# Kernel optimization log

Measured on AMD Instinct MI355X. Metric: run time of the kernel, lower is better.

The kernel has to match this reference:

```python
import jax, jax.numpy as jnp
import numpy as np

# ---- static config (matches init_kwargs) ----
B, CIN, H, W = 32, 64, 32, 32
CO, K, G, PAD = 64, 7, 8, 3
R_RAMP = 3.0            # ramp size R
Z_INIT = 4.0            # initial adaptive-span value
MAXSZ = W // 2          # adaptive_mask max_size = image_size/2 = 16
CPG = CO // G           # channels per group


def _unfold(t, k):
    # torch x.unfold(2,k,1).unfold(3,k,1): [B,C,Hp,Wp] -> [B,C,Ho,Wo,kh,kw]
    ho = t.shape[2] - k + 1
    wo = t.shape[3] - k + 1
    return jnp.stack(
        [jnp.stack([t[:, :, i:i + ho, j:j + wo] for j in range(k)], axis=-1)
         for i in range(k)], axis=-2)


def _adaptive_mask(current_val):
    # AdaptiveMask.forward applied to [B,G,CPG,H,W]; x.shape[-1] == W.
    # one_d_mask[g, i] is the soft value written on 'ring' i (rows i and W-1-i,
    # columns spanning the ring interval) of a WxW mask.
    template = jnp.linspace(1.0 - MAXSZ, 0.0, MAXSZ)            # [MAXSZ]
    om = (template[None, :] + current_val * MAXSZ) / R_RAMP + 1.0
    om = jnp.clip(om, 0.0, 1.0)                                  # [G, MAXSZ]
    # (slice [-(W//2):] is identity since MAXSZ == W//2)
    i = jnp.arange(W)
    r = jnp.minimum(i, W - 1 - i)                                # ring index per row
    top = i <= (W - 1 - i)
    lo = jnp.where(top, r, r + 1)    # bottom row of ring misses its leftmost col
    hi = W - 1 - r
    c = jnp.arange(W)
    in_ring = (c[None, :] >= lo[:, None]) & (c[None, :] <= hi[:, None])  # [W,W]
    vals = om[:, r]                                              # [G, W]
    return jnp.where(in_ring[None, :, :], vals[:, :, None], 1.0)  # [G,W,W]


def setup_inputs() -> dict:
    key = jax.random.key(0)
    ks = jax.random.split(key, 6)
    x = jax.random.normal(ks[0], (B, CIN, H, W), dtype=jnp.float32)
    fan_out_std = np.sqrt(2.0 / CO).astype(np.float32)  # kaiming fan_out, 1x1 conv
    w_q = jax.random.normal(ks[1], (CO, CIN), dtype=jnp.float32) * fan_out_std
    w_k = jax.random.normal(ks[2], (CO, CIN), dtype=jnp.float32) * fan_out_std
    w_v = jax.random.normal(ks[3], (CO, CIN), dtype=jnp.float32) * fan_out_std
    rel_h = jax.random.normal(ks[4], (CO // 2, 1, 1, K, 1), dtype=jnp.float32)
    rel_w = jax.random.normal(ks[5], (CO // 2, 1, 1, 1, K), dtype=jnp.float32)
    current_val = jnp.full((G, 1), Z_INIT, dtype=jnp.float32)
    return {"x": x, "w_q": w_q, "w_k": w_k, "w_v": w_v,
            "rel_h": rel_h, "rel_w": rel_w, "current_val": current_val}


def reference(x, w_q, w_k, w_v, rel_h, rel_w, current_val):
    q = jnp.einsum('bchw,oc->bohw', x, w_q)                       # [B,CO,H,W]
    xp = jnp.pad(x, ((0, 0), (0, 0), (PAD, PAD), (PAD, PAD)))
    k = jnp.einsum('bchw,oc->bohw', xp, w_k)
    v = jnp.einsum('bchw,oc->bohw', xp, w_v)
    k = _unfold(k, K)                                             # [B,CO,H,W,K,K]
    v = _unfold(v, K)
    k_h, k_w = jnp.split(k, 2, axis=1)
    k = jnp.concatenate([k_h + rel_h, k_w + rel_w], axis=1)
    k = k.reshape(B, G, CPG, H, W, K * K)
    v = v.reshape(B, G, CPG, H, W, K * K)
    q = q.reshape(B, G, CPG, H, W, 1)
    scores = jnp.sum(q * k, axis=2)                               # [B,G,H,W,K*K]
    attn = jax.nn.softmax(scores, axis=-1)
    out = jnp.sum(attn[:, :, None] * v, axis=-1)                  # [B,G,CPG,H,W]
    mask = _adaptive_mask(current_val)                            # [G,W,W]
    return out * mask[None, :, None, :, :]
```

## Files before the change

### kernel.cpp

```cpp
#include <hip/hip_runtime.h>

#define BB    32
#define CINc  64
#define HHc   32
#define WWc   32
#define COc   64
#define KSc   7
#define GGc   8
#define PADc  3
#define CPGc  8
#define NPIX  (HHc * WWc)
#define TILEH 8
#define HALOH (TILEH + 6)
#define HALOW (WWc + 6)
#define NPOS  (HALOH * HALOW)

typedef _Float16 half2v __attribute__((ext_vector_type(2)));

#if defined(__has_builtin)
#if __has_builtin(__builtin_amdgcn_fdot2)
#define HAVE_FDOT2 1
#endif
#endif

__global__ __launch_bounds__(256, 6) void fused_kernel(
    const float* __restrict__ x,
    const float* __restrict__ wq,
    const float* __restrict__ wk,
    const float* __restrict__ wv,
    const float* __restrict__ rel_h,
    const float* __restrict__ rel_w,
    const float* __restrict__ cv,
    float* __restrict__ out)
{
    __shared__ __attribute__((aligned(16))) float4 kpl[NPOS];
    __shared__ __attribute__((aligned(16))) float4 vpl0[NPOS];
    __shared__ __attribute__((aligned(16))) float4 vpl1[NPOS];

    const int bi   = blockIdx.x;
    const int xcd  = bi & 7;
    const int sIdx = bi >> 3;
    const int im   = sIdx >> 5;
    const int j    = sIdx & 31;
    const int b    = im * 8 + xcd;
    const int g    = j >> 2;
    const int tile = j & 3;
    const int o0   = g * CPGc;
    const int tid  = threadIdx.x;

    const int y0  = tile * TILEH - PADc;
    const int yv0 = (y0 < 0) ? 0 : y0;
    const int yv1 = (y0 + HALOH - 1 > HHc - 1) ? (HHc - 1) : (y0 + HALOH - 1);
    const int nvp = ((yv1 - yv0) + 1) << 5;
    const int r0  = yv0 - y0;
    const float* xb = x + (size_t)b * CINc * NPIX;

    {
        const float4 z = {0.f, 0.f, 0.f, 0.f};
        for (int p = tid; p < NPOS; p += 256) {
            kpl[p] = z; vpl0[p] = z; vpl1[p] = z;
        }
    }
    __syncthreads();

#pragma unroll 1
    for (int i = tid; i < nvp; i += 256) {
        const int row = i >> 5;
        const int xx  = i & 31;
        const int y   = yv0 + row;
        const float* xp = xb + y * WWc + xx;

        float ak[CPGc], av[CPGc];
#pragma unroll
        for (int oi = 0; oi < CPGc; ++oi) { ak[oi] = 0.f; av[oi] = 0.f; }

        for (int c0 = 0; c0 < CINc; c0 += 8) {
            float xv[8];
#pragma unroll
            for (int jj = 0; jj < 8; ++jj)
                xv[jj] = xp[(c0 + jj) * NPIX];
#pragma unroll
            for (int oi = 0; oi < CPGc; ++oi) {
                const float* wkr = wk + (o0 + oi) * CINc + c0;
                const float* wvr = wv + (o0 + oi) * CINc + c0;
#pragma unroll
                for (int jj = 0; jj < 8; ++jj) {
                    ak[oi] = fmaf(xv[jj], wkr[jj], ak[oi]);
                    av[oi] = fmaf(xv[jj], wvr[jj], av[oi]);
                }
            }
        }

        const int p = (r0 + row) * HALOW + (xx + PADc);
        float4 kst;
        half2v* kp = (half2v*)&kst;
#pragma unroll
        for (int jj = 0; jj < 4; ++jj)
            kp[jj] = half2v{(_Float16)ak[2 * jj], (_Float16)ak[2 * jj + 1]};
        kpl[p]  = kst;
        vpl0[p] = (float4){av[0], av[1], av[2], av[3]};
        vpl1[p] = (float4){av[4], av[5], av[6], av[7]};
    }

    const int w  = tid & 31;
    const int lh = tid >> 5;
    const int h  = tile * TILEH + lh;
    const int poff = h * WWc + w;

    float q[CPGc];
#pragma unroll
    for (int oi = 0; oi < CPGc; ++oi) q[oi] = 0.f;

    for (int c0 = 0; c0 < CINc; c0 += 8) {
        float xv[8];
#pragma unroll
        for (int jj = 0; jj < 8; ++jj)
            xv[jj] = xb[(c0 + jj) * NPIX + poff];
#pragma unroll
        for (int oi = 0; oi < CPGc; ++oi) {
            const float* wqr = wq + (o0 + oi) * CINc + c0;
#pragma unroll
            for (int jj = 0; jj < 8; ++jj)
                q[oi] = fmaf(xv[jj], wqr[jj], q[oi]);
        }
    }

#if HAVE_FDOT2
    half2v q2[4];
#pragma unroll
    for (int jj = 0; jj < 4; ++jj)
        q2[jj] = half2v{(_Float16)q[2 * jj], (_Float16)q[2 * jj + 1]};
#endif

    const bool use_h = (g < 4);
    const float* relp = use_h ? (rel_h + o0 * KSc) : (rel_w + (o0 - 32) * KSc);
    float qrel[KSc];
#pragma unroll
    for (int tt = 0; tt < KSc; ++tt) {
        float s = 0.f;
#pragma unroll
        for (int oi = 0; oi < CPGc; ++oi)
            s = fmaf(q[oi], relp[oi * KSc + tt], s);
        qrel[tt] = s;
    }

    __syncthreads();

    float den = 0.f;
    float acc[CPGc];
#pragma unroll
    for (int oi = 0; oi < CPGc; ++oi) acc[oi] = 0.f;

#pragma unroll
    for (int ki = 0; ki < KSc; ++ki) {
        const int rbase = (lh + ki) * HALOW + w;
#pragma unroll
        for (int kj = 0; kj < KSc; ++kj) {
            const int p = rbase + kj;
            const float4 kraw = kpl[p];
            const float4 v0   = vpl0[p];
            const float4 v1   = vpl1[p];

            float s = use_h ? qrel[ki] : qrel[kj];
#if HAVE_FDOT2
            const half2v* kh = (const half2v*)&kraw;
            s = __builtin_amdgcn_fdot2(q2[0], kh[0], s, false);
            s = __builtin_amdgcn_fdot2(q2[1], kh[1], s, false);
            s = __builtin_amdgcn_fdot2(q2[2], kh[2], s, false);
            s = __builtin_amdgcn_fdot2(q2[3], kh[3], s, false);
#else
            const half2v* kh = (const half2v*)&kraw;
#pragma unroll
            for (int jj = 0; jj < 4; ++jj) {
                s = fmaf(q[2 * jj],     (float)kh[jj].x, s);
                s = fmaf(q[2 * jj + 1], (float)kh[jj].y, s);
            }
#endif
            const float e = __expf(s);
            den += e;
            acc[0] = fmaf(e, v0.x, acc[0]); acc[1] = fmaf(e, v0.y, acc[1]);
            acc[2] = fmaf(e, v0.z, acc[2]); acc[3] = fmaf(e, v0.w, acc[3]);
            acc[4] = fmaf(e, v1.x, acc[4]); acc[5] = fmaf(e, v1.y, acc[5]);
            acc[6] = fmaf(e, v1.z, acc[6]); acc[7] = fmaf(e, v1.w, acc[7]);
        }
    }

    const int  r  = min(h, HHc - 1 - h);
    const int  lo = (h <= HHc - 1 - h) ? r : r + 1;
    const int  hi = HHc - 1 - r;
    const bool in_ring = (w >= lo) && (w <= hi);
    const float cvg = cv[g];
    float om = ((float)r - 15.0f + cvg * 16.0f) * (1.0f / 3.0f) + 1.0f;
    om = fminf(fmaxf(om, 0.0f), 1.0f);
    const float maskv = in_ring ? om : 1.0f;
    const float scale = maskv / den;

    float* ob = out + ((size_t)b * COc + o0) * NPIX + poff;
#pragma unroll
    for (int oi = 0; oi < CPGc; ++oi)
        ob[(size_t)oi * NPIX] = acc[oi] * scale;
}

extern "C" void kernel_launch(void* const* d_in, const int* in_sizes, int n_in,
                              void* d_out, int out_size, void* d_ws, size_t ws_size,
                              hipStream_t stream) {
    const float* x     = (const float*)d_in[0];
    const float* wq    = (const float*)d_in[1];
    const float* wk    = (const float*)d_in[2];
    const float* wv    = (const float*)d_in[3];
    const float* rel_h = (const float*)d_in[4];
    const float* rel_w = (const float*)d_in[5];
    const float* cv    = (const float*)d_in[6];
    float* out = (float*)d_out;

    fused_kernel<<<1024, 256, 0, stream>>>(x, wq, wk, wv, rel_h, rel_w, cv, out);
}
```

Measured before the change: 106.7 us.

## Process whole image per block to drop halo recompute of K/V projections

Each block now covers a full 32x32 image for one (batch, group) pair with 1024 threads, instead of an 8-row tile plus a 3-row halo. Each thread computes its pixel's Q, K and V projections in a single pass, so halo rows are no longer recomputed and the zeroed halo shared buffer goes away. Out-of-bounds neighbours are handled by clamping indices and masking the dot product and value accumulation. The trade-off is fewer blocks (256), which may leave compute units underused, plus extra select instructions in the inner loop.

```diff
diff --git a/kernel.cpp b/kernel.cpp
--- a/kernel.cpp
+++ b/kernel.cpp
@@ -10,10 +10,6 @@
 #define PADc  3
 #define CPGc  8
 #define NPIX  (HHc * WWc)
-#define TILEH 8
-#define HALOH (TILEH + 6)
-#define HALOW (WWc + 6)
-#define NPOS  (HALOH * HALOW)
 
 typedef _Float16 half2v __attribute__((ext_vector_type(2)));
 
@@ -23,7 +19,7 @@
 #endif
 #endif
 
-__global__ __launch_bounds__(256, 6) void fused_kernel(
+__global__ __launch_bounds__(1024, 4) void fused_kernel(
     const float* __restrict__ x,
     const float* __restrict__ wq,
     const float* __restrict__ wk,
@@ -33,103 +29,63 @@
     const float* __restrict__ cv,
     float* __restrict__ out)
 {
-    __shared__ __attribute__((aligned(16))) float4 kpl[NPOS];
-    __shared__ __attribute__((aligned(16))) float4 vpl0[NPOS];
-    __shared__ __attribute__((aligned(16))) float4 vpl1[NPOS];
+    __shared__ __attribute__((aligned(16))) float4 kpl[NPIX];
+    __shared__ __attribute__((aligned(16))) float4 vpl0[NPIX];
+    __shared__ __attribute__((aligned(16))) float4 vpl1[NPIX];
 
-    const int bi   = blockIdx.x;
-    const int xcd  = bi & 7;
-    const int sIdx = bi >> 3;
-    const int im   = sIdx >> 5;
-    const int j    = sIdx & 31;
-    const int b    = im * 8 + xcd;
-    const int g    = j >> 2;
-    const int tile = j & 3;
-    const int o0   = g * CPGc;
-    const int tid  = threadIdx.x;
+    const int bi  = blockIdx.x;
+    const int xcd = bi & 7;
+    const int t   = bi >> 3;
+    const int im  = t & 3;
+    const int g   = t >> 2;
+    const int b   = im * 8 + xcd;
+    const int o0  = g * CPGc;
+    const int tid = threadIdx.x;
+    const int w   = tid & 31;
+    const int h   = tid >> 5;
 
-    const int y0  = tile * TILEH - PADc;
-    const int yv0 = (y0 < 0) ? 0 : y0;
-    const int yv1 = (y0 + HALOH - 1 > HHc - 1) ? (HHc - 1) : (y0 + HALOH - 1);
-    const int nvp = ((yv1 - yv0) + 1) << 5;
-    const int r0  = yv0 - y0;
     const float* xb = x + (size_t)b * CINc * NPIX;
+    const float* xp = xb + tid;
+
+    float ak[CPGc], av[CPGc], aq[CPGc];
+#pragma unroll
+    for (int oi = 0; oi < CPGc; ++oi) { ak[oi] = 0.f; av[oi] = 0.f; aq[oi] = 0.f; }
+
+    for (int c0 = 0; c0 < CINc; c0 += 8) {
+        float xv[8];
+#pragma unroll
+        for (int jj = 0; jj < 8; ++jj)
+            xv[jj] = xp[(c0 + jj) * NPIX];
+#pragma unroll
+        for (int oi = 0; oi < CPGc; ++oi) {
+            const float* wkr = wk + (o0 + oi) * CINc + c0;
+            const float* wvr = wv + (o0 + oi) * CINc + c0;
+            const float* wqr = wq + (o0 + oi) * CINc + c0;
+#pragma unroll
+            for (int jj = 0; jj < 8; ++jj) {
+                ak[oi] = fmaf(xv[jj], wkr[jj], ak[oi]);
+                av[oi] = fmaf(xv[jj], wvr[jj], av[oi]);
+                aq[oi] = fmaf(xv[jj], wqr[jj], aq[oi]);
+            }
+        }
+    }
 
     {
-        const float4 z = {0.f, 0.f, 0.f, 0.f};
-        for (int p = tid; p < NPOS; p += 256) {
-            kpl[p] = z; vpl0[p] = z; vpl1[p] = z;
-        }
-    }
-    __syncthreads();
-
-#pragma unroll 1
-    for (int i = tid; i < nvp; i += 256) {
-        const int row = i >> 5;
-        const int xx  = i & 31;
-        const int y   = yv0 + row;
-        const float* xp = xb + y * WWc + xx;
-
-        float ak[CPGc], av[CPGc];
-#pragma unroll
-        for (int oi = 0; oi < CPGc; ++oi) { ak[oi] = 0.f; av[oi] = 0.f; }
-
-        for (int c0 = 0; c0 < CINc; c0 += 8) {
-            float xv[8];
-#pragma unroll
-            for (int jj = 0; jj < 8; ++jj)
-                xv[jj] = xp[(c0 + jj) * NPIX];
-#pragma unroll
-            for (int oi = 0; oi < CPGc; ++oi) {
-                const float* wkr = wk + (o0 + oi) * CINc + c0;
-                const float* wvr = wv + (o0 + oi) * CINc + c0;
-#pragma unroll
-                for (int jj = 0; jj < 8; ++jj) {
-                    ak[oi] = fmaf(xv[jj], wkr[jj], ak[oi]);
-                    av[oi] = fmaf(xv[jj], wvr[jj], av[oi]);
-                }
-            }
-        }
-
-        const int p = (r0 + row) * HALOW + (xx + PADc);
         float4 kst;
         half2v* kp = (half2v*)&kst;
 #pragma unroll
         for (int jj = 0; jj < 4; ++jj)
             kp[jj] = half2v{(_Float16)ak[2 * jj], (_Float16)ak[2 * jj + 1]};
-        kpl[p]  = kst;
-        vpl0[p] = (float4){av[0], av[1], av[2], av[3]};
-        vpl1[p] = (float4){av[4], av[5], av[6], av[7]};
-    }
-
-    const int w  = tid & 31;
-    const int lh = tid >> 5;
-    const int h  = tile * TILEH + lh;
-    const int poff = h * WWc + w;
-
-    float q[CPGc];
-#pragma unroll
-    for (int oi = 0; oi < CPGc; ++oi) q[oi] = 0.f;
-
-    for (int c0 = 0; c0 < CINc; c0 += 8) {
-        float xv[8];
-#pragma unroll
-        for (int jj = 0; jj < 8; ++jj)
-            xv[jj] = xb[(c0 + jj) * NPIX + poff];
-#pragma unroll
-        for (int oi = 0; oi < CPGc; ++oi) {
-            const float* wqr = wq + (o0 + oi) * CINc + c0;
-#pragma unroll
-            for (int jj = 0; jj < 8; ++jj)
-                q[oi] = fmaf(xv[jj], wqr[jj], q[oi]);
-        }
+        kpl[tid]  = kst;
+        vpl0[tid] = (float4){av[0], av[1], av[2], av[3]};
+        vpl1[tid] = (float4){av[4], av[5], av[6], av[7]};
     }
 
 #if HAVE_FDOT2
     half2v q2[4];
 #pragma unroll
     for (int jj = 0; jj < 4; ++jj)
-        q2[jj] = half2v{(_Float16)q[2 * jj], (_Float16)q[2 * jj + 1]};
+        q2[jj] = half2v{(_Float16)aq[2 * jj], (_Float16)aq[2 * jj + 1]};
 #endif
 
     const bool use_h = (g < 4);
@@ -140,11 +96,20 @@
         float s = 0.f;
 #pragma unroll
         for (int oi = 0; oi < CPGc; ++oi)
-            s = fmaf(q[oi], relp[oi * KSc + tt], s);
+            s = fmaf(aq[oi], relp[oi * KSc + tt], s);
         qrel[tt] = s;
     }
 
     __syncthreads();
+
+    int  xcl[KSc];
+    bool xin[KSc];
+#pragma unroll
+    for (int kj = 0; kj < KSc; ++kj) {
+        const int xx = w + kj - PADc;
+        xin[kj] = (xx >= 0) && (xx < WWc);
+        xcl[kj] = min(max(xx, 0), WWc - 1);
+    }
 
     float den = 0.f;
     float acc[CPGc];
@@ -153,35 +118,40 @@
 
 #pragma unroll
     for (int ki = 0; ki < KSc; ++ki) {
-        const int rbase = (lh + ki) * HALOW + w;
+        const int y   = h + ki - PADc;
+        const bool yin = (y >= 0) && (y < HHc);
+        const int base = min(max(y, 0), HHc - 1) * WWc;
 #pragma unroll
         for (int kj = 0; kj < KSc; ++kj) {
-            const int p = rbase + kj;
+            const int p = base + xcl[kj];
             const float4 kraw = kpl[p];
             const float4 v0   = vpl0[p];
             const float4 v1   = vpl1[p];
+            const bool in = yin && xin[kj];
 
-            float s = use_h ? qrel[ki] : qrel[kj];
+            float d = 0.f;
 #if HAVE_FDOT2
             const half2v* kh = (const half2v*)&kraw;
-            s = __builtin_amdgcn_fdot2(q2[0], kh[0], s, false);
-            s = __builtin_amdgcn_fdot2(q2[1], kh[1], s, false);
-            s = __builtin_amdgcn_fdot2(q2[2], kh[2], s, false);
-            s = __builtin_amdgcn_fdot2(q2[3], kh[3], s, false);
+            d = __builtin_amdgcn_fdot2(q2[0], kh[0], d, false);
+            d = __builtin_amdgcn_fdot2(q2[1], kh[1], d, false);
+            d = __builtin_amdgcn_fdot2(q2[2], kh[2], d, false);
+            d = __builtin_amdgcn_fdot2(q2[3], kh[3], d, false);
 #else
             const half2v* kh = (const half2v*)&kraw;
 #pragma unroll
             for (int jj = 0; jj < 4; ++jj) {
-                s = fmaf(q[2 * jj],     (float)kh[jj].x, s);
-                s = fmaf(q[2 * jj + 1], (float)kh[jj].y, s);
+                d = fmaf(aq[2 * jj],     (float)kh[jj].x, d);
+                d = fmaf(aq[2 * jj + 1], (float)kh[jj].y, d);
             }
 #endif
+            const float s = (use_h ? qrel[ki] : qrel[kj]) + (in ? d : 0.f);
             const float e = __expf(s);
             den += e;
-            acc[0] = fmaf(e, v0.x, acc[0]); acc[1] = fmaf(e, v0.y, acc[1]);
-            acc[2] = fmaf(e, v0.z, acc[2]); acc[3] = fmaf(e, v0.w, acc[3]);
-            acc[4] = fmaf(e, v1.x, acc[4]); acc[5] = fmaf(e, v1.y, acc[5]);
-            acc[6] = fmaf(e, v1.z, acc[6]); acc[7] = fmaf(e, v1.w, acc[7]);
+            const float ev = in ? e : 0.f;
+            acc[0] = fmaf(ev, v0.x, acc[0]); acc[1] = fmaf(ev, v0.y, acc[1]);
+            acc[2] = fmaf(ev, v0.z, acc[2]); acc[3] = fmaf(ev, v0.w, acc[3]);
+            acc[4] = fmaf(ev, v1.x, acc[4]); acc[5] = fmaf(ev, v1.y, acc[5]);
+            acc[6] = fmaf(ev, v1.z, acc[6]); acc[7] = fmaf(ev, v1.w, acc[7]);
         }
     }
 
@@ -195,7 +165,7 @@
     const float maskv = in_ring ? om : 1.0f;
     const float scale = maskv / den;
 
-    float* ob = out + ((size_t)b * COc + o0) * NPIX + poff;
+    float* ob = out + ((size_t)b * COc + o0) * NPIX + tid;
 #pragma unroll
     for (int oi = 0; oi < CPGc; ++oi)
         ob[(size_t)oi * NPIX] = acc[oi] * scale;
@@ -213,5 +183,5 @@
     const float* cv    = (const float*)d_in[6];
     float* out = (float*)d_out;
 
-    fused_kernel<<<1024, 256, 0, stream>>>(x, wq, wk, wv, rel_h, rel_w, cv, out);
+    fused_kernel<<<256, 1024, 0, stream>>>(x, wq, wk, wv, rel_h, rel_w, cv, out);
 }
```

Result: faster. 103.7 us (-2.8%).
